# Kernel tuning notes

Hardware: AMD Instinct MI355X
Metric: run time of the kernel (lower is better)

Reference implementation:

```python
import jax, jax.numpy as jnp
import numpy as np

EMBED_DIM = 1024
CONTEXT_DIM = 768
NUM_HEADS = 16
HEAD_DIM = EMBED_DIM // NUM_HEADS
B, N, M = 8, 4096, 77


def setup_inputs() -> dict:
    key = jax.random.key(0)
    ks = jax.random.split(key, 12)
    s_in = 1.0 / np.sqrt(EMBED_DIM)
    s_ctx = 1.0 / np.sqrt(CONTEXT_DIM)
    x = jax.random.normal(ks[0], (B, N, EMBED_DIM), dtype=jnp.float32)
    context = jax.random.normal(ks[1], (B, M, CONTEXT_DIM), dtype=jnp.float32)
    # realistic padding mask: each example has a random valid prefix length in [1, M]
    lengths = jax.random.randint(ks[2], (B,), 1, M + 1)
    context_mask = jnp.arange(M)[None, :] < lengths[:, None]  # (B, M) bool
    Wq = jax.random.uniform(ks[3], (EMBED_DIM, EMBED_DIM), jnp.float32, -s_in, s_in)
    bq = jax.random.uniform(ks[4], (EMBED_DIM,), jnp.float32, -s_in, s_in)
    Wk = jax.random.uniform(ks[5], (CONTEXT_DIM, EMBED_DIM), jnp.float32, -s_ctx, s_ctx)
    bk = jax.random.uniform(ks[6], (EMBED_DIM,), jnp.float32, -s_ctx, s_ctx)
    Wv = jax.random.uniform(ks[7], (CONTEXT_DIM, EMBED_DIM), jnp.float32, -s_ctx, s_ctx)
    bv = jax.random.uniform(ks[8], (EMBED_DIM,), jnp.float32, -s_ctx, s_ctx)
    Wo = jax.random.uniform(ks[9], (EMBED_DIM, EMBED_DIM), jnp.float32, -s_in, s_in)
    bo = jax.random.uniform(ks[10], (EMBED_DIM,), jnp.float32, -s_in, s_in)
    return {"x": x, "context": context, "context_mask": context_mask,
            "Wq": Wq, "bq": bq, "Wk": Wk, "bk": bk, "Wv": Wv, "bv": bv,
            "Wo": Wo, "bo": bo}


def reference(x, context, context_mask, Wq, bq, Wk, bk, Wv, bv, Wo, bo):
    H, d = NUM_HEADS, HEAD_DIM
    scale = d ** -0.5
    Bx, Nx, _ = x.shape
    Mx = context.shape[1]
    # projections
    q = (x @ Wq + bq).reshape(Bx, Nx, H, d).transpose(0, 2, 1, 3)        # (B,H,N,d)
    k = (context @ Wk + bk).reshape(Bx, Mx, H, d).transpose(0, 2, 1, 3)  # (B,H,M,d)
    v = (context @ Wv + bv).reshape(Bx, Mx, H, d).transpose(0, 2, 1, 3)  # (B,H,M,d)
    # scores with padding mask
    attn = jnp.einsum('bhnd,bhmd->bhnm', q, k) * scale                   # (B,H,N,M)
    attn = jnp.where(context_mask[:, None, None, :], attn, -jnp.inf)
    attn = jax.nn.softmax(attn, axis=-1)
    out = jnp.einsum('bhnm,bhmd->bhnd', attn, v)                          # (B,H,N,d)
    out = out.transpose(0, 2, 1, 3).reshape(Bx, Nx, H * d)                # (B,N,E)
    return out @ Wo + bo
```

## Files before the change

### kernel.cpp

```cpp
#include <hip/hip_runtime.h>

typedef __bf16 bf16x8 __attribute__((ext_vector_type(8)));
typedef float f32x4 __attribute__((ext_vector_type(4)));

#define EMB 1024
#define CTXD 768
#define NH 16
#define HD 64
#define BB 8
#define NN 4096
#define MM 77
#define MPAD 96

static __device__ __forceinline__ unsigned short f2bf(float f) {
    unsigned u = __builtin_bit_cast(unsigned, f);
    u += 0x7FFFu + ((u >> 16) & 1u);
    return (unsigned short)(u >> 16);
}

__global__ void cast_f32_to_bf16(const float* __restrict__ in,
                                 unsigned short* __restrict__ out, int n8) {
    for (int i = blockIdx.x * blockDim.x + threadIdx.x; i < n8;
         i += gridDim.x * blockDim.x) {
        float4 v0 = ((const float4*)in)[2 * i];
        float4 v1 = ((const float4*)in)[2 * i + 1];
        union { unsigned short u[8]; int4 v; } r;
        r.u[0] = f2bf(v0.x); r.u[1] = f2bf(v0.y);
        r.u[2] = f2bf(v0.z); r.u[3] = f2bf(v0.w);
        r.u[4] = f2bf(v1.x); r.u[5] = f2bf(v1.y);
        r.u[6] = f2bf(v1.z); r.u[7] = f2bf(v1.w);
        ((int4*)out)[i] = r.v;
    }
}

struct PrepArgs {
    const float* wsrc[4];
    unsigned short* wdst[4];
    const float* ctx;
    unsigned short* cbf;
    const unsigned char* mask;
    int* lengths;
    int4* kvzero;
};
__global__ void prep_kernel(PrepArgs pa) {
    const int z = blockIdx.z;
    const int tx = threadIdx.x, ty = threadIdx.y;
    const int tid = ty * 32 + tx;
    if (z < 4) {
        __shared__ float t[32][33];
        int R = (z < 2) ? 1024 : 768, C = 1024;
        int r0 = blockIdx.y * 32;
        if (r0 >= R) return;
        const float* W = pa.wsrc[z];
        unsigned short* Wt = pa.wdst[z];
        int c0 = blockIdx.x * 32;
#pragma unroll
        for (int i = 0; i < 32; i += 8)
            t[ty + i][tx] = W[(size_t)(r0 + ty + i) * C + c0 + tx];
        __syncthreads();
#pragma unroll
        for (int i = 0; i < 32; i += 8)
            Wt[(size_t)(c0 + ty + i) * R + r0 + tx] = f2bf(t[tx][ty + i]);
    } else if (z == 4) {
        int fid = blockIdx.y * 32 + blockIdx.x;
        int i = fid * 256 + tid;
        if (i >= 640 * CTXD / 8) return;
        int row = (i * 8) / CTXD;
        union { unsigned short u[8]; int4 v; } r;
        if (row < BB * MM) {
            float4 v0 = ((const float4*)pa.ctx)[2 * i];
            float4 v1 = ((const float4*)pa.ctx)[2 * i + 1];
            r.u[0] = f2bf(v0.x); r.u[1] = f2bf(v0.y);
            r.u[2] = f2bf(v0.z); r.u[3] = f2bf(v0.w);
            r.u[4] = f2bf(v1.x); r.u[5] = f2bf(v1.y);
            r.u[6] = f2bf(v1.z); r.u[7] = f2bf(v1.w);
        } else {
            r.v = make_int4(0, 0, 0, 0);
        }
        ((int4*)pa.cbf)[i] = r.v;
    } else {
        int fid = blockIdx.y * 32 + blockIdx.x;
        int i = fid * 256 + tid;
        if (i < 196608) pa.kvzero[i] = make_int4(0, 0, 0, 0);
        if (fid == 1023 && tid < 64) {
            int ln = tid;
            int anyOdd = 0, anyF = 0;
            for (int k = ln; k < BB * MM; k += 64) {
                unsigned char v = pa.mask[k];
                if (v == 0x80u || v == 0x3Fu) anyF = 1;
                if ((k & 3) && v) anyOdd = 1;
            }
            anyF = __any(anyF); anyOdd = __any(anyOdd);
            int layout = anyF ? 2 : (anyOdd ? 1 : 0);
            int b = ln >> 3, j = ln & 7, cnt = 0;
            for (int m = j; m < MM; m += 8) {
                int idx = b * MM + m;
                int valid;
                if (layout == 1)      valid = pa.mask[idx] != 0;
                else if (layout == 0) valid = ((const int*)pa.mask)[idx] != 0;
                else                  valid = ((const float*)pa.mask)[idx] != 0.0f;
                cnt += valid ? 1 : 0;
            }
            cnt += __shfl_xor(cnt, 1, 64);
            cnt += __shfl_xor(cnt, 2, 64);
            cnt += __shfl_xor(cnt, 4, 64);
            if (j == 0) pa.lengths[b] = cnt;
        }
    }
}

template <int MODE>
__global__ __launch_bounds__(512, 2) void gemm256_kernel(
    const unsigned short* __restrict__ A, const unsigned short* __restrict__ Bt,
    const float* __restrict__ bias, void* __restrict__ Cout,
    int M, int N, int K) {
    __shared__ unsigned short lds[4][2][256 * 32];
    const int tid = threadIdx.x, wv = tid >> 6, ln = tid & 63;
    const int numN = N >> 8;
    int bid = blockIdx.x;
    const int nwg = (M >> 8) * numN;
    if ((nwg & 7) == 0) { int cpx = nwg >> 3; bid = (bid & 7) * cpx + (bid >> 3); }
    const int nt_ = bid % numN, mt = bid / numN;
    const int m0 = mt << 8, n0 = nt_ << 8;
    const int wr = wv >> 2, wc = wv & 3;
    const int NT = K >> 5;

    const int srow = wv * 16 + (ln >> 2);
    const int sslot = ln & 3;

    auto stageA = [&](int t) {
#pragma unroll
        for (int half = 0; half < 2; ++half) {
            int row = half * 128 + srow;
            int gc = sslot ^ ((row >> 1) & 3);
            __builtin_amdgcn_global_load_lds(
                (const __attribute__((address_space(1))) void*)(
                    A + (size_t)(m0 + row) * K + (t << 5) + gc * 8),
                (__attribute__((address_space(3))) void*)(
                    &lds[t & 3][0][(half * 128 + wv * 16) * 32]),
                16, 0, 0);
        }
    };
    auto stageB = [&](int t) {
#pragma unroll
        for (int half = 0; half < 2; ++half) {
            int row = half * 128 + srow;
            int gc = sslot ^ ((row >> 1) & 3);
            __builtin_amdgcn_global_load_lds(
                (const __attribute__((address_space(1))) void*)(
                    Bt + (size_t)(n0 + row) * K + (t << 5) + gc * 8),
                (__attribute__((address_space(3))) void*)(
                    &lds[t & 3][1][(half * 128 + wv * 16) * 32]),
                16, 0, 0);
        }
    };
    auto readA = [&](const unsigned short* As, int i) -> bf16x8 {
        int arow = wr * 128 + i * 16 + (ln & 15);
        int aslot = (ln >> 4) ^ ((arow >> 1) & 3);
        return *(const bf16x8*)(As + arow * 32 + aslot * 8);
    };
    auto readB = [&](const unsigned short* Bs, int j) -> bf16x8 {
        int brow = wc * 64 + j * 16 + (ln & 15);
        int bslot = (ln >> 4) ^ ((brow >> 1) & 3);
        return *(const bf16x8*)(Bs + brow * 32 + bslot * 8);
    };

    f32x4 acc[8][4] = {};

    stageA(0); stageB(0); stageA(1); stageB(1); stageA(2); stageB(2);
    asm volatile("s_waitcnt vmcnt(8)" ::: "memory");
    __builtin_amdgcn_sched_barrier(0);
    __builtin_amdgcn_s_barrier();

#pragma unroll 4
    for (int t = 0; t < NT; ++t) {
        const unsigned short* As = lds[t & 3][0];
        const unsigned short* Bs = lds[t & 3][1];
        if (t + 3 < NT) stageA(t + 3);
        bf16x8 bfr[4], af[4];
#pragma unroll
        for (int j = 0; j < 4; ++j) bfr[j] = readB(Bs, j);
#pragma unroll
        for (int i = 0; i < 4; ++i) af[i] = readA(As, i);
        __builtin_amdgcn_s_barrier();
        __builtin_amdgcn_s_setprio(1);
#pragma unroll
        for (int i = 0; i < 4; ++i)
#pragma unroll
            for (int j = 0; j < 4; ++j)
                acc[i][j] = __builtin_amdgcn_mfma_f32_16x16x32_bf16(
                    af[i], bfr[j], acc[i][j], 0, 0, 0);
        __builtin_amdgcn_s_setprio(0);
        __builtin_amdgcn_s_barrier();
        if (t + 3 < NT) stageB(t + 3);
#pragma unroll
        for (int i = 0; i < 4; ++i) af[i] = readA(As, i + 4);
        __builtin_amdgcn_s_barrier();
        __builtin_amdgcn_s_setprio(1);
#pragma unroll
        for (int i = 0; i < 4; ++i)
#pragma unroll
            for (int j = 0; j < 4; ++j)
                acc[i + 4][j] = __builtin_amdgcn_mfma_f32_16x16x32_bf16(
                    af[i], bfr[j], acc[i + 4][j], 0, 0, 0);
        __builtin_amdgcn_s_setprio(0);
        if (t < NT - 1) {
            if (t + 3 < NT)      { asm volatile("s_waitcnt vmcnt(8)" ::: "memory"); }
            else if (t + 2 < NT) { asm volatile("s_waitcnt vmcnt(4)" ::: "memory"); }
            else                 { asm volatile("s_waitcnt vmcnt(0)" ::: "memory"); }
            __builtin_amdgcn_sched_barrier(0);
        }
        __builtin_amdgcn_s_barrier();
    }

    float bvals[4];
#pragma unroll
    for (int j = 0; j < 4; ++j)
        bvals[j] = bias[n0 + wc * 64 + j * 16 + (ln & 15)];
#pragma unroll
    for (int i = 0; i < 8; ++i)
#pragma unroll
        for (int j = 0; j < 4; ++j)
#pragma unroll
            for (int r = 0; r < 4; ++r) {
                int row = m0 + wr * 128 + i * 16 + (ln >> 4) * 4 + r;
                int col = n0 + wc * 64 + j * 16 + (ln & 15);
                float v = acc[i][j][r] + bvals[j];
                if constexpr (MODE == 0)
                    ((unsigned short*)Cout)[(size_t)row * N + col] = f2bf(v);
                else
                    ((float*)Cout)[(size_t)row * N + col] = v;
            }
}

static __device__ __forceinline__ void stage_tile(
    const unsigned short* __restrict__ G, int ldg, unsigned short* lds,
    int r0, int kt, int wv, int ln) {
    int rown = ln >> 2;
    int koff = (ln & 3) * 8;
#pragma unroll
    for (int r = 0; r < 2; ++r) {
        int cw = wv * 2 + r;
        const unsigned short* src =
            G + (size_t)(r0 + cw * 16 + rown) * ldg + kt + koff;
        __builtin_amdgcn_global_load_lds(
            (const __attribute__((address_space(1))) void*)src,
            (__attribute__((address_space(3))) void*)(lds + cw * 512),
            16, 0, 0);
    }
}

__global__ __launch_bounds__(256) void gemm_kv_kernel(
    const unsigned short* __restrict__ Cbf,
    const unsigned short* __restrict__ Wk_t, const float* __restrict__ bk,
    unsigned short* __restrict__ Kw,
    const unsigned short* __restrict__ Wv_t, const float* __restrict__ bv,
    unsigned short* __restrict__ Vtw) {
    const int M = 640, N = 1024, K = CTXD;
    __shared__ unsigned short As[128 * 32];
    __shared__ unsigned short Bs[128 * 32];
    const int tid = threadIdx.x, wv = tid >> 6, ln = tid & 63;
    int bid = blockIdx.x;
    const bool isV = bid >= 40;
    if (isV) bid -= 40;
    const unsigned short* Bt = isV ? Wv_t : Wk_t;
    const float* bias = isV ? bv : bk;
    const int numN = N >> 7;
    { int cpx = 5; bid = (bid & 7) * cpx + (bid >> 3); }
    const int nt = bid % numN, mt = bid / numN;
    const int m0 = mt << 7, n0 = nt << 7;
    const int wr = wv >> 1, wc = wv & 1;

    f32x4 acc[4][4] = {};
    for (int kt = 0; kt < K; kt += 32) {
        __syncthreads();
        stage_tile(Cbf, K, As, m0, kt, wv, ln);
        stage_tile(Bt, K, Bs, n0, kt, wv, ln);
        __syncthreads();
        bf16x8 af[4], bfr[4];
#pragma unroll
        for (int i = 0; i < 4; ++i)
            af[i] = *(const bf16x8*)(As + (wr * 64 + i * 16 + (ln & 15)) * 32 +
                                     (ln >> 4) * 8);
#pragma unroll
        for (int j = 0; j < 4; ++j)
            bfr[j] = *(const bf16x8*)(Bs + (wc * 64 + j * 16 + (ln & 15)) * 32 +
                                      (ln >> 4) * 8);
#pragma unroll
        for (int i = 0; i < 4; ++i)
#pragma unroll
            for (int j = 0; j < 4; ++j)
                acc[i][j] = __builtin_amdgcn_mfma_f32_16x16x32_bf16(
                    af[i], bfr[j], acc[i][j], 0, 0, 0);
    }

    float bvals[4];
#pragma unroll
    for (int j = 0; j < 4; ++j)
        bvals[j] = bias[n0 + wc * 64 + j * 16 + (ln & 15)];

#pragma unroll
    for (int i = 0; i < 4; ++i) {
#pragma unroll
        for (int j = 0; j < 4; ++j) {
#pragma unroll
            for (int r = 0; r < 4; ++r) {
                int row = m0 + wr * 64 + i * 16 + (ln >> 4) * 4 + r;
                int col = n0 + wc * 64 + j * 16 + (ln & 15);
                float v = acc[i][j][r] + bvals[j];
                if (row < BB * MM) {
                    int bb = row / MM, m = row - bb * MM;
                    int hh = col >> 6, d = col & 63;
                    if (!isV)
                        Kw[((size_t)(bb * NH + hh) * MPAD + m) * HD + d] = f2bf(v);
                    else
                        Vtw[((size_t)(bb * NH + hh) * HD + d) * MPAD + m] = f2bf(v);
                }
            }
        }
    }
}

__global__ __launch_bounds__(256, 3) void attn_kernel(
    const unsigned short* __restrict__ Q, const unsigned short* __restrict__ Kw,
    const unsigned short* __restrict__ Vt, const int* __restrict__ lengths,
    unsigned short* __restrict__ Out) {
    const int bh = blockIdx.y;
    const int b = bh >> 4, h = bh & 15;
    const int q0 = blockIdx.x * 128;
    const int tid = threadIdx.x, wv = tid >> 6, ln = tid & 63;
    const int len = lengths[b];
    const int kscnt = (len + 31) >> 5;

    __shared__ unsigned short Ps[128][104];

    const unsigned short* Ksrc = Kw + (size_t)bh * (MPAD * HD);
    const unsigned short* Vsrc = Vt + (size_t)bh * (HD * MPAD);

    bf16x8 aq[2][2];
#pragma unroll
    for (int qi = 0; qi < 2; ++qi) {
        const int qr = q0 + wv * 32 + qi * 16 + (ln & 15);
        const unsigned short* qptr =
            Q + (size_t)(b * NN + qr) * EMB + h * HD + (ln >> 4) * 8;
        aq[qi][0] = *(const bf16x8*)(qptr);
        aq[qi][1] = *(const bf16x8*)(qptr + 32);
    }

    bf16x8 vf[3][4];
#pragma unroll
    for (int j = 0; j < 4; ++j)
        vf[0][j] = *(const bf16x8*)(Vsrc + (j * 16 + (ln & 15)) * MPAD +
                                    (ln >> 4) * 8);
    if (kscnt > 1) {
#pragma unroll
        for (int j = 0; j < 4; ++j)
            vf[1][j] = *(const bf16x8*)(Vsrc + (j * 16 + (ln & 15)) * MPAD + 32 +
                                        (ln >> 4) * 8);
    }
    if (kscnt > 2) {
#pragma unroll
        for (int j = 0; j < 4; ++j)
            vf[2][j] = *(const bf16x8*)(Vsrc + (j * 16 + (ln & 15)) * MPAD + 64 +
                                        (ln >> 4) * 8);
    }

    f32x4 s[2][5] = {};
#pragma unroll
    for (int t = 0; t < 5; ++t) {
        if (t * 16 < len) {
            const unsigned short* kp =
                Ksrc + (t * 16 + (ln & 15)) * HD + (ln >> 4) * 8;
            bf16x8 k0 = *(const bf16x8*)(kp);
            bf16x8 k1 = *(const bf16x8*)(kp + 32);
#pragma unroll
            for (int qi = 0; qi < 2; ++qi) {
                s[qi][t] = __builtin_amdgcn_mfma_f32_16x16x32_bf16(
                    aq[qi][0], k0, s[qi][t], 0, 0, 0);
                s[qi][t] = __builtin_amdgcn_mfma_f32_16x16x32_bf16(
                    aq[qi][1], k1, s[qi][t], 0, 0, 0);
            }
        }
    }

    const float scale = 0.125f;
    float mx[2][4], sum[2][4];
#pragma unroll
    for (int qi = 0; qi < 2; ++qi)
#pragma unroll
        for (int r = 0; r < 4; ++r) { mx[qi][r] = -1e30f; sum[qi][r] = 0.f; }
#pragma unroll
    for (int t = 0; t < 5; ++t) {
        int m = t * 16 + (ln & 15);
        bool valid = m < len;
#pragma unroll
        for (int qi = 0; qi < 2; ++qi)
#pragma unroll
            for (int r = 0; r < 4; ++r) {
                float v = valid ? s[qi][t][r] * scale : -1e30f;
                s[qi][t][r] = v;
                mx[qi][r] = fmaxf(mx[qi][r], v);
            }
    }
#pragma unroll
    for (int d = 1; d < 16; d <<= 1)
#pragma unroll
        for (int qi = 0; qi < 2; ++qi)
#pragma unroll
            for (int r = 0; r < 4; ++r)
                mx[qi][r] = fmaxf(mx[qi][r], __shfl_xor(mx[qi][r], d, 64));
#pragma unroll
    for (int t = 0; t < 5; ++t)
#pragma unroll
        for (int qi = 0; qi < 2; ++qi)
#pragma unroll
            for (int r = 0; r < 4; ++r) {
                float p = __expf(s[qi][t][r] - mx[qi][r]);
                s[qi][t][r] = p;
                sum[qi][r] += p;
            }
#pragma unroll
    for (int d = 1; d < 16; d <<= 1)
#pragma unroll
        for (int qi = 0; qi < 2; ++qi)
#pragma unroll
            for (int r = 0; r < 4; ++r)
                sum[qi][r] += __shfl_xor(sum[qi][r], d, 64);

    float rinv[2][4];
#pragma unroll
    for (int qi = 0; qi < 2; ++qi)
#pragma unroll
        for (int r = 0; r < 4; ++r) rinv[qi][r] = 1.0f / sum[qi][r];

#pragma unroll
    for (int t = 0; t < 6; ++t)
#pragma unroll
        for (int qi = 0; qi < 2; ++qi)
#pragma unroll
            for (int r = 0; r < 4; ++r) {
                int row = wv * 32 + qi * 16 + (ln >> 4) * 4 + r;
                float v = (t < 5) ? s[qi][t][r] * rinv[qi][r] : 0.0f;
                Ps[row][t * 16 + (ln & 15)] = f2bf(v);
            }

    f32x4 o[2][4] = {};
    for (int ks = 0; ks < kscnt; ++ks) {
#pragma unroll
        for (int qi = 0; qi < 2; ++qi) {
            bf16x8 pf = *(const bf16x8*)(&Ps[wv * 32 + qi * 16 + (ln & 15)]
                                            [ks * 32 + (ln >> 4) * 8]);
#pragma unroll
            for (int j = 0; j < 4; ++j)
                o[qi][j] = __builtin_amdgcn_mfma_f32_16x16x32_bf16(
                    vf[ks][j], pf, o[qi][j], 0, 0, 0);
        }
    }

#pragma unroll
    for (int qi = 0; qi < 2; ++qi) {
        const int qrow = q0 + wv * 32 + qi * 16 + (ln & 15);
        unsigned short* obase =
            Out + (size_t)(b * NN + qrow) * EMB + h * HD + (ln >> 4) * 4;
#pragma unroll
        for (int j = 0; j < 4; ++j) {
            union { unsigned short u[4]; unsigned long long ll; } pk;
#pragma unroll
            for (int r = 0; r < 4; ++r) pk.u[r] = f2bf(o[qi][j][r]);
            *(unsigned long long*)(obase + j * 16) = pk.ll;
        }
    }
}

extern "C" void kernel_launch(void* const* d_in, const int* in_sizes, int n_in,
                              void* d_out, int out_size, void* d_ws, size_t ws_size,
                              hipStream_t stream) {
    const float* x    = (const float*)d_in[0];
    const float* ctx  = (const float*)d_in[1];
    const unsigned char* cmask = (const unsigned char*)d_in[2];
    const float* Wq = (const float*)d_in[3];
    const float* bq = (const float*)d_in[4];
    const float* Wk = (const float*)d_in[5];
    const float* bk = (const float*)d_in[6];
    const float* Wv = (const float*)d_in[7];
    const float* bv = (const float*)d_in[8];
    const float* Wo = (const float*)d_in[9];
    const float* bo = (const float*)d_in[10];

    char* ws = (char*)d_ws;
    unsigned short* Xbf   = (unsigned short*)(ws);
    unsigned short* Wq_t  = (unsigned short*)(ws + 67108864);
    unsigned short* Wo_t  = (unsigned short*)(ws + 69206016);
    unsigned short* Wk_t  = (unsigned short*)(ws + 71303168);
    unsigned short* Wv_t  = (unsigned short*)(ws + 72876032);
    unsigned short* Cbf   = (unsigned short*)(ws + 74448896);
    unsigned short* Kw    = (unsigned short*)(ws + 75431936);
    unsigned short* Vtw   = (unsigned short*)(ws + 77004800);
    int* lengths          = (int*)(ws + 78577664);
    unsigned short* Qb    = (unsigned short*)d_out;

    PrepArgs pa;
    pa.wsrc[0] = Wq; pa.wsrc[1] = Wo; pa.wsrc[2] = Wk; pa.wsrc[3] = Wv;
    pa.wdst[0] = Wq_t; pa.wdst[1] = Wo_t; pa.wdst[2] = Wk_t; pa.wdst[3] = Wv_t;
    pa.ctx = ctx; pa.cbf = Cbf; pa.mask = cmask; pa.lengths = lengths;
    pa.kvzero = (int4*)Kw;
    prep_kernel<<<dim3(32, 32, 6), dim3(32, 8), 0, stream>>>(pa);

    cast_f32_to_bf16<<<2048, 256, 0, stream>>>(x, Xbf, (BB * NN * EMB) / 8);

    gemm256_kernel<0><<<512, 512, 0, stream>>>(Xbf, Wq_t, bq, Qb, 32768, 1024, 1024);
    gemm_kv_kernel<<<80, 256, 0, stream>>>(Cbf, Wk_t, bk, Kw, Wv_t, bv, Vtw);

    attn_kernel<<<dim3(32, 128), 256, 0, stream>>>(Qb, Kw, Vtw, lengths, Xbf);

    gemm256_kernel<1><<<512, 512, 0, stream>>>(Xbf, Wo_t, bo, d_out, 32768, 1024, 1024);
}
```

Baseline: 293.5 us.

## Fold x cast into prep kernel and merge Q and KV GEMMs into one launch

The fp32-to-bf16 cast of x becomes extra z-slices of the prep kernel. The Q projection GEMM and the small K/V projection GEMM now share one 592-block launch, with the first 80 blocks running the K/V path on 8 waves. This removes two kernel launches and their tail gaps. It also lowers the s_waitcnt vmcnt thresholds in the pipelined GEMMs from 8/4 to 4/2, which waits on more outstanding prefetches than the three-stage-ahead pipeline needs and may reduce load/compute overlap.

```diff
diff --git a/kernel.cpp b/kernel.cpp
--- a/kernel.cpp
+++ b/kernel.cpp
@@ -18,21 +18,6 @@
     return (unsigned short)(u >> 16);
 }
 
-__global__ void cast_f32_to_bf16(const float* __restrict__ in,
-                                 unsigned short* __restrict__ out, int n8) {
-    for (int i = blockIdx.x * blockDim.x + threadIdx.x; i < n8;
-         i += gridDim.x * blockDim.x) {
-        float4 v0 = ((const float4*)in)[2 * i];
-        float4 v1 = ((const float4*)in)[2 * i + 1];
-        union { unsigned short u[8]; int4 v; } r;
-        r.u[0] = f2bf(v0.x); r.u[1] = f2bf(v0.y);
-        r.u[2] = f2bf(v0.z); r.u[3] = f2bf(v0.w);
-        r.u[4] = f2bf(v1.x); r.u[5] = f2bf(v1.y);
-        r.u[6] = f2bf(v1.z); r.u[7] = f2bf(v1.w);
-        ((int4*)out)[i] = r.v;
-    }
-}
-
 struct PrepArgs {
     const float* wsrc[4];
     unsigned short* wdst[4];
@@ -41,6 +26,8 @@
     const unsigned char* mask;
     int* lengths;
     int4* kvzero;
+    const float* x;
+    unsigned short* xbf;
 };
 __global__ void prep_kernel(PrepArgs pa) {
     const int z = blockIdx.z;
@@ -78,7 +65,7 @@
             r.v = make_int4(0, 0, 0, 0);
         }
         ((int4*)pa.cbf)[i] = r.v;
-    } else {
+    } else if (z == 5) {
         int fid = blockIdx.y * 32 + blockIdx.x;
         int i = fid * 256 + tid;
         if (i < 196608) pa.kvzero[i] = make_int4(0, 0, 0, 0);
@@ -106,13 +93,217 @@
             cnt += __shfl_xor(cnt, 4, 64);
             if (j == 0) pa.lengths[b] = cnt;
         }
+    } else {
+        int i = ((z - 6) * 1024 + blockIdx.y * 32 + blockIdx.x) * 256 + tid;
+        float4 v0 = ((const float4*)pa.x)[2 * i];
+        float4 v1 = ((const float4*)pa.x)[2 * i + 1];
+        union { unsigned short u[8]; int4 v; } r;
+        r.u[0] = f2bf(v0.x); r.u[1] = f2bf(v0.y);
+        r.u[2] = f2bf(v0.z); r.u[3] = f2bf(v0.w);
+        r.u[4] = f2bf(v1.x); r.u[5] = f2bf(v1.y);
+        r.u[6] = f2bf(v1.z); r.u[7] = f2bf(v1.w);
+        ((int4*)pa.xbf)[i] = r.v;
     }
 }
 
-template <int MODE>
+__global__ __launch_bounds__(512, 2) void gemm_q_kv(
+    const unsigned short* __restrict__ Xbf, const unsigned short* __restrict__ Wq_t,
+    const float* __restrict__ bq, unsigned short* __restrict__ Qb,
+    const unsigned short* __restrict__ Cbf,
+    const unsigned short* __restrict__ Wk_t, const float* __restrict__ bk,
+    unsigned short* __restrict__ Kw,
+    const unsigned short* __restrict__ Wv_t, const float* __restrict__ bv,
+    unsigned short* __restrict__ Vtw) {
+    __shared__ unsigned short lds[4][2][256 * 32];
+    const int tid = threadIdx.x, wv = tid >> 6, ln = tid & 63;
+    int bid = blockIdx.x;
+
+    if (bid < 80) {
+        const bool isV = bid >= 40;
+        if (isV) bid -= 40;
+        const unsigned short* Bt = isV ? Wv_t : Wk_t;
+        const float* bias = isV ? bv : bk;
+        { int cpx = 5; bid = (bid & 7) * cpx + (bid >> 3); }
+        const int nt = bid & 7, mt = bid >> 3;
+        const int m0 = mt << 7, n0 = nt << 7;
+        const int wr = wv >> 2, wc = wv & 3;
+        unsigned short* As = &lds[0][0][0];
+        unsigned short* Bs = &lds[0][1][0];
+
+        f32x4 acc[4][2] = {};
+        const int rown = ln >> 2, koff = (ln & 3) * 8;
+        for (int kt = 0; kt < CTXD; kt += 32) {
+            __syncthreads();
+            __builtin_amdgcn_global_load_lds(
+                (const __attribute__((address_space(1))) void*)(
+                    Cbf + (size_t)(m0 + wv * 16 + rown) * CTXD + kt + koff),
+                (__attribute__((address_space(3))) void*)(As + wv * 512),
+                16, 0, 0);
+            __builtin_amdgcn_global_load_lds(
+                (const __attribute__((address_space(1))) void*)(
+                    Bt + (size_t)(n0 + wv * 16 + rown) * CTXD + kt + koff),
+                (__attribute__((address_space(3))) void*)(Bs + wv * 512),
+                16, 0, 0);
+            __syncthreads();
+            bf16x8 af[4], bfr[2];
+#pragma unroll
+            for (int i = 0; i < 4; ++i)
+                af[i] = *(const bf16x8*)(As + (wr * 64 + i * 16 + (ln & 15)) * 32 +
+                                         (ln >> 4) * 8);
+#pragma unroll
+            for (int j = 0; j < 2; ++j)
+                bfr[j] = *(const bf16x8*)(Bs + (wc * 32 + j * 16 + (ln & 15)) * 32 +
+                                          (ln >> 4) * 8);
+#pragma unroll
+            for (int i = 0; i < 4; ++i)
+#pragma unroll
+                for (int j = 0; j < 2; ++j)
+                    acc[i][j] = __builtin_amdgcn_mfma_f32_16x16x32_bf16(
+                        af[i], bfr[j], acc[i][j], 0, 0, 0);
+        }
+
+        float bvals[2];
+#pragma unroll
+        for (int j = 0; j < 2; ++j)
+            bvals[j] = bias[n0 + wc * 32 + j * 16 + (ln & 15)];
+#pragma unroll
+        for (int i = 0; i < 4; ++i)
+#pragma unroll
+            for (int j = 0; j < 2; ++j)
+#pragma unroll
+                for (int r = 0; r < 4; ++r) {
+                    int row = m0 + wr * 64 + i * 16 + (ln >> 4) * 4 + r;
+                    int col = n0 + wc * 32 + j * 16 + (ln & 15);
+                    float v = acc[i][j][r] + bvals[j];
+                    if (row < BB * MM) {
+                        int bb = row / MM, m = row - bb * MM;
+                        int hh = col >> 6, d = col & 63;
+                        if (!isV)
+                            Kw[((size_t)(bb * NH + hh) * MPAD + m) * HD + d] = f2bf(v);
+                        else
+                            Vtw[((size_t)(bb * NH + hh) * HD + d) * MPAD + m] = f2bf(v);
+                    }
+                }
+        return;
+    }
+
+    bid -= 80;
+    const int M = 32768, N = 1024, K = 1024;
+    const int numN = N >> 8;
+    const int nwg = (M >> 8) * numN;
+    { int cpx = nwg >> 3; bid = (bid & 7) * cpx + (bid >> 3); }
+    const int nt_ = bid % numN, mt = bid / numN;
+    const int m0 = mt << 8, n0 = nt_ << 8;
+    const int wr = wv >> 2, wc = wv & 3;
+    const int NT = K >> 5;
+
+    const int srow = wv * 16 + (ln >> 2);
+    const int sslot = ln & 3;
+
+    auto stageA = [&](int t) {
+#pragma unroll
+        for (int half = 0; half < 2; ++half) {
+            int row = half * 128 + srow;
+            int gc = sslot ^ ((row >> 1) & 3);
+            __builtin_amdgcn_global_load_lds(
+                (const __attribute__((address_space(1))) void*)(
+                    Xbf + (size_t)(m0 + row) * K + (t << 5) + gc * 8),
+                (__attribute__((address_space(3))) void*)(
+                    &lds[t & 3][0][(half * 128 + wv * 16) * 32]),
+                16, 0, 0);
+        }
+    };
+    auto stageB = [&](int t) {
+#pragma unroll
+        for (int half = 0; half < 2; ++half) {
+            int row = half * 128 + srow;
+            int gc = sslot ^ ((row >> 1) & 3);
+            __builtin_amdgcn_global_load_lds(
+                (const __attribute__((address_space(1))) void*)(
+                    Wq_t + (size_t)(n0 + row) * K + (t << 5) + gc * 8),
+                (__attribute__((address_space(3))) void*)(
+                    &lds[t & 3][1][(half * 128 + wv * 16) * 32]),
+                16, 0, 0);
+        }
+    };
+    auto readA = [&](const unsigned short* As, int i) -> bf16x8 {
+        int arow = wr * 128 + i * 16 + (ln & 15);
+        int aslot = (ln >> 4) ^ ((arow >> 1) & 3);
+        return *(const bf16x8*)(As + arow * 32 + aslot * 8);
+    };
+    auto readB = [&](const unsigned short* Bs, int j) -> bf16x8 {
+        int brow = wc * 64 + j * 16 + (ln & 15);
+        int bslot = (ln >> 4) ^ ((brow >> 1) & 3);
+        return *(const bf16x8*)(Bs + brow * 32 + bslot * 8);
+    };
+
+    f32x4 acc[8][4] = {};
+
+    stageA(0); stageB(0); stageA(1); stageB(1); stageA(2); stageB(2);
+    asm volatile("s_waitcnt vmcnt(8)" ::: "memory");
+    __builtin_amdgcn_sched_barrier(0);
+    __builtin_amdgcn_s_barrier();
+
+#pragma unroll 4
+    for (int t = 0; t < NT; ++t) {
+        const unsigned short* As = lds[t & 3][0];
+        const unsigned short* Bs = lds[t & 3][1];
+        if (t + 3 < NT) stageA(t + 3);
+        bf16x8 bfr[4], af[4];
+#pragma unroll
+        for (int j = 0; j < 4; ++j) bfr[j] = readB(Bs, j);
+#pragma unroll
+        for (int i = 0; i < 4; ++i) af[i] = readA(As, i);
+        __builtin_amdgcn_s_barrier();
+        __builtin_amdgcn_s_setprio(1);
+#pragma unroll
+        for (int i = 0; i < 4; ++i)
+#pragma unroll
+            for (int j = 0; j < 4; ++j)
+                acc[i][j] = __builtin_amdgcn_mfma_f32_16x16x32_bf16(
+                    af[i], bfr[j], acc[i][j], 0, 0, 0);
+        __builtin_amdgcn_s_setprio(0);
+        __builtin_amdgcn_s_barrier();
+        if (t + 3 < NT) stageB(t + 3);
+#pragma unroll
+        for (int i = 0; i < 4; ++i) af[i] = readA(As, i + 4);
+        __builtin_amdgcn_s_barrier();
+        __builtin_amdgcn_s_setprio(1);
+#pragma unroll
+        for (int i = 0; i < 4; ++i)
+#pragma unroll
+            for (int j = 0; j < 4; ++j)
+                acc[i + 4][j] = __builtin_amdgcn_mfma_f32_16x16x32_bf16(
+                    af[i], bfr[j], acc[i + 4][j], 0, 0, 0);
+        __builtin_amdgcn_s_setprio(0);
+        if (t < NT - 1) {
+            if (t + 3 < NT)      { asm volatile("s_waitcnt vmcnt(4)" ::: "memory"); }
+            else if (t + 2 < NT) { asm volatile("s_waitcnt vmcnt(2)" ::: "memory"); }
+            else                 { asm volatile("s_waitcnt vmcnt(0)" ::: "memory"); }
+            __builtin_amdgcn_sched_barrier(0);
+        }
+        __builtin_amdgcn_s_barrier();
+    }
+
+    float bvals[4];
+#pragma unroll
+    for (int j = 0; j < 4; ++j)
+        bvals[j] = bq[n0 + wc * 64 + j * 16 + (ln & 15)];
+#pragma unroll
+    for (int i = 0; i < 8; ++i)
+#pragma unroll
+        for (int j = 0; j < 4; ++j)
+#pragma unroll
+            for (int r = 0; r < 4; ++r) {
+                int row = m0 + wr * 128 + i * 16 + (ln >> 4) * 4 + r;
+                int col = n0 + wc * 64 + j * 16 + (ln & 15);
+                Qb[(size_t)row * N + col] = f2bf(acc[i][j][r] + bvals[j]);
+            }
+}
+
 __global__ __launch_bounds__(512, 2) void gemm256_kernel(
     const unsigned short* __restrict__ A, const unsigned short* __restrict__ Bt,
-    const float* __restrict__ bias, void* __restrict__ Cout,
+    const float* __restrict__ bias, float* __restrict__ Cout,
     int M, int N, int K) {
     __shared__ unsigned short lds[4][2][256 * 32];
     const int tid = threadIdx.x, wv = tid >> 6, ln = tid & 63;
@@ -205,8 +396,8 @@
                     af[i], bfr[j], acc[i + 4][j], 0, 0, 0);
         __builtin_amdgcn_s_setprio(0);
         if (t < NT - 1) {
-            if (t + 3 < NT)      { asm volatile("s_waitcnt vmcnt(8)" ::: "memory"); }
-            else if (t + 2 < NT) { asm volatile("s_waitcnt vmcnt(4)" ::: "memory"); }
+            if (t + 3 < NT)      { asm volatile("s_waitcnt vmcnt(4)" ::: "memory"); }
+            else if (t + 2 < NT) { asm volatile("s_waitcnt vmcnt(2)" ::: "memory"); }
             else                 { asm volatile("s_waitcnt vmcnt(0)" ::: "memory"); }
             __builtin_amdgcn_sched_barrier(0);
         }
@@ -225,100 +416,8 @@
             for (int r = 0; r < 4; ++r) {
                 int row = m0 + wr * 128 + i * 16 + (ln >> 4) * 4 + r;
                 int col = n0 + wc * 64 + j * 16 + (ln & 15);
-                float v = acc[i][j][r] + bvals[j];
-                if constexpr (MODE == 0)
-                    ((unsigned short*)Cout)[(size_t)row * N + col] = f2bf(v);
-                else
-                    ((float*)Cout)[(size_t)row * N + col] = v;
-            }
-}
-
-static __device__ __forceinline__ void stage_tile(
-    const unsigned short* __restrict__ G, int ldg, unsigned short* lds,
-    int r0, int kt, int wv, int ln) {
-    int rown = ln >> 2;
-    int koff = (ln & 3) * 8;
-#pragma unroll
-    for (int r = 0; r < 2; ++r) {
-        int cw = wv * 2 + r;
-        const unsigned short* src =
-            G + (size_t)(r0 + cw * 16 + rown) * ldg + kt + koff;
-        __builtin_amdgcn_global_load_lds(
-            (const __attribute__((address_space(1))) void*)src,
-            (__attribute__((address_space(3))) void*)(lds + cw * 512),
-            16, 0, 0);
-    }
-}
-
-__global__ __launch_bounds__(256) void gemm_kv_kernel(
-    const unsigned short* __restrict__ Cbf,
-    const unsigned short* __restrict__ Wk_t, const float* __restrict__ bk,
-    unsigned short* __restrict__ Kw,
-    const unsigned short* __restrict__ Wv_t, const float* __restrict__ bv,
-    unsigned short* __restrict__ Vtw) {
-    const int M = 640, N = 1024, K = CTXD;
-    __shared__ unsigned short As[128 * 32];
-    __shared__ unsigned short Bs[128 * 32];
-    const int tid = threadIdx.x, wv = tid >> 6, ln = tid & 63;
-    int bid = blockIdx.x;
-    const bool isV = bid >= 40;
-    if (isV) bid -= 40;
-    const unsigned short* Bt = isV ? Wv_t : Wk_t;
-    const float* bias = isV ? bv : bk;
-    const int numN = N >> 7;
-    { int cpx = 5; bid = (bid & 7) * cpx + (bid >> 3); }
-    const int nt = bid % numN, mt = bid / numN;
-    const int m0 = mt << 7, n0 = nt << 7;
-    const int wr = wv >> 1, wc = wv & 1;
-
-    f32x4 acc[4][4] = {};
-    for (int kt = 0; kt < K; kt += 32) {
-        __syncthreads();
-        stage_tile(Cbf, K, As, m0, kt, wv, ln);
-        stage_tile(Bt, K, Bs, n0, kt, wv, ln);
-        __syncthreads();
-        bf16x8 af[4], bfr[4];
-#pragma unroll
-        for (int i = 0; i < 4; ++i)
-            af[i] = *(const bf16x8*)(As + (wr * 64 + i * 16 + (ln & 15)) * 32 +
-                                     (ln >> 4) * 8);
-#pragma unroll
-        for (int j = 0; j < 4; ++j)
-            bfr[j] = *(const bf16x8*)(Bs + (wc * 64 + j * 16 + (ln & 15)) * 32 +
-                                      (ln >> 4) * 8);
-#pragma unroll
-        for (int i = 0; i < 4; ++i)
-#pragma unroll
-            for (int j = 0; j < 4; ++j)
-                acc[i][j] = __builtin_amdgcn_mfma_f32_16x16x32_bf16(
-                    af[i], bfr[j], acc[i][j], 0, 0, 0);
-    }
-
-    float bvals[4];
-#pragma unroll
-    for (int j = 0; j < 4; ++j)
-        bvals[j] = bias[n0 + wc * 64 + j * 16 + (ln & 15)];
-
-#pragma unroll
-    for (int i = 0; i < 4; ++i) {
-#pragma unroll
-        for (int j = 0; j < 4; ++j) {
-#pragma unroll
-            for (int r = 0; r < 4; ++r) {
-                int row = m0 + wr * 64 + i * 16 + (ln >> 4) * 4 + r;
-                int col = n0 + wc * 64 + j * 16 + (ln & 15);
-                float v = acc[i][j][r] + bvals[j];
-                if (row < BB * MM) {
-                    int bb = row / MM, m = row - bb * MM;
-                    int hh = col >> 6, d = col & 63;
-                    if (!isV)
-                        Kw[((size_t)(bb * NH + hh) * MPAD + m) * HD + d] = f2bf(v);
-                    else
-                        Vtw[((size_t)(bb * NH + hh) * HD + d) * MPAD + m] = f2bf(v);
-                }
-            }
-        }
-    }
+                Cout[(size_t)row * N + col] = acc[i][j][r] + bvals[j];
+            }
 }
 
 __global__ __launch_bounds__(256, 3) void attn_kernel(
@@ -504,14 +603,14 @@
     pa.wdst[0] = Wq_t; pa.wdst[1] = Wo_t; pa.wdst[2] = Wk_t; pa.wdst[3] = Wv_t;
     pa.ctx = ctx; pa.cbf = Cbf; pa.mask = cmask; pa.lengths = lengths;
     pa.kvzero = (int4*)Kw;
-    prep_kernel<<<dim3(32, 32, 6), dim3(32, 8), 0, stream>>>(pa);
-
-    cast_f32_to_bf16<<<2048, 256, 0, stream>>>(x, Xbf, (BB * NN * EMB) / 8);
-
-    gemm256_kernel<0><<<512, 512, 0, stream>>>(Xbf, Wq_t, bq, Qb, 32768, 1024, 1024);
-    gemm_kv_kernel<<<80, 256, 0, stream>>>(Cbf, Wk_t, bk, Kw, Wv_t, bv, Vtw);
+    pa.x = x; pa.xbf = Xbf;
+    prep_kernel<<<dim3(32, 32, 22), dim3(32, 8), 0, stream>>>(pa);
+
+    gemm_q_kv<<<592, 512, 0, stream>>>(Xbf, Wq_t, bq, Qb,
+                                       Cbf, Wk_t, bk, Kw, Wv_t, bv, Vtw);
 
     attn_kernel<<<dim3(32, 128), 256, 0, stream>>>(Qb, Kw, Vtw, lengths, Xbf);
 
-    gemm256_kernel<1><<<512, 512, 0, stream>>>(Xbf, Wo_t, bo, d_out, 32768, 1024, 1024);
+    gemm256_kernel<<<512, 512, 0, stream>>>(Xbf, Wo_t, bo, (float*)d_out,
+                                            32768, 1024, 1024);
 }
```

After: 265.0 us. -9.7%, faster.

## Shrink GEMM tiles to 128x128, merge Q and KV GEMMs, fold x cast into prep

Applied to the files above, without the earlier changes.

The 256x256, 512-thread GEMM is replaced by a 128x128, 256-thread variant with a 4-stage LDS pipeline. The Q projection and the small K/V projection now run in one launch, and the fp32-to-bf16 cast of x moves into the prep kernel as extra z-slices. This removes two launches and lets the K/V blocks overlap the Q GEMM, but the smaller tiles lower per-block arithmetic intensity and raise global and LDS traffic per FLOP.

```diff
diff --git a/kernel.cpp b/kernel.cpp
--- a/kernel.cpp
+++ b/kernel.cpp
@@ -18,21 +18,6 @@
     return (unsigned short)(u >> 16);
 }
 
-__global__ void cast_f32_to_bf16(const float* __restrict__ in,
-                                 unsigned short* __restrict__ out, int n8) {
-    for (int i = blockIdx.x * blockDim.x + threadIdx.x; i < n8;
-         i += gridDim.x * blockDim.x) {
-        float4 v0 = ((const float4*)in)[2 * i];
-        float4 v1 = ((const float4*)in)[2 * i + 1];
-        union { unsigned short u[8]; int4 v; } r;
-        r.u[0] = f2bf(v0.x); r.u[1] = f2bf(v0.y);
-        r.u[2] = f2bf(v0.z); r.u[3] = f2bf(v0.w);
-        r.u[4] = f2bf(v1.x); r.u[5] = f2bf(v1.y);
-        r.u[6] = f2bf(v1.z); r.u[7] = f2bf(v1.w);
-        ((int4*)out)[i] = r.v;
-    }
-}
-
 struct PrepArgs {
     const float* wsrc[4];
     unsigned short* wdst[4];
@@ -41,6 +26,8 @@
     const unsigned char* mask;
     int* lengths;
     int4* kvzero;
+    const float* x;
+    unsigned short* xbf;
 };
 __global__ void prep_kernel(PrepArgs pa) {
     const int z = blockIdx.z;
@@ -53,11 +40,11 @@
         if (r0 >= R) return;
         const float* W = pa.wsrc[z];
         unsigned short* Wt = pa.wdst[z];
+#pragma unroll
+        for (int i = 0; i < 32; i += 8)
+            t[ty + i][tx] = W[(size_t)(r0 + ty + i) * C + blockIdx.x * 32 + tx];
+        __syncthreads();
         int c0 = blockIdx.x * 32;
-#pragma unroll
-        for (int i = 0; i < 32; i += 8)
-            t[ty + i][tx] = W[(size_t)(r0 + ty + i) * C + c0 + tx];
-        __syncthreads();
 #pragma unroll
         for (int i = 0; i < 32; i += 8)
             Wt[(size_t)(c0 + ty + i) * R + r0 + tx] = f2bf(t[tx][ty + i]);
@@ -78,7 +65,7 @@
             r.v = make_int4(0, 0, 0, 0);
         }
         ((int4*)pa.cbf)[i] = r.v;
-    } else {
+    } else if (z == 5) {
         int fid = blockIdx.y * 32 + blockIdx.x;
         int i = fid * 256 + tid;
         if (i < 196608) pa.kvzero[i] = make_int4(0, 0, 0, 0);
@@ -106,23 +93,31 @@
             cnt += __shfl_xor(cnt, 4, 64);
             if (j == 0) pa.lengths[b] = cnt;
         }
+    } else {
+        int i = ((z - 6) * 1024 + blockIdx.y * 32 + blockIdx.x) * 256 + tid;
+        float4 v0 = ((const float4*)pa.x)[2 * i];
+        float4 v1 = ((const float4*)pa.x)[2 * i + 1];
+        union { unsigned short u[8]; int4 v; } r;
+        r.u[0] = f2bf(v0.x); r.u[1] = f2bf(v0.y);
+        r.u[2] = f2bf(v0.z); r.u[3] = f2bf(v0.w);
+        r.u[4] = f2bf(v1.x); r.u[5] = f2bf(v1.y);
+        r.u[6] = f2bf(v1.z); r.u[7] = f2bf(v1.w);
+        ((int4*)pa.xbf)[i] = r.v;
     }
 }
 
 template <int MODE>
-__global__ __launch_bounds__(512, 2) void gemm256_kernel(
+static __device__ __forceinline__ void gemm128_core(
     const unsigned short* __restrict__ A, const unsigned short* __restrict__ Bt,
     const float* __restrict__ bias, void* __restrict__ Cout,
-    int M, int N, int K) {
-    __shared__ unsigned short lds[4][2][256 * 32];
-    const int tid = threadIdx.x, wv = tid >> 6, ln = tid & 63;
-    const int numN = N >> 8;
-    int bid = blockIdx.x;
-    const int nwg = (M >> 8) * numN;
+    int M, int N, int K, int bid, int wv, int ln,
+    unsigned short (*lds)[2][128 * 32]) {
+    const int numN = N >> 7;
+    const int nwg = (M >> 7) * numN;
     if ((nwg & 7) == 0) { int cpx = nwg >> 3; bid = (bid & 7) * cpx + (bid >> 3); }
     const int nt_ = bid % numN, mt = bid / numN;
-    const int m0 = mt << 8, n0 = nt_ << 8;
-    const int wr = wv >> 2, wc = wv & 3;
+    const int m0 = mt << 7, n0 = nt_ << 7;
+    const int wr = wv >> 1, wc = wv & 1;
     const int NT = K >> 5;
 
     const int srow = wv * 16 + (ln >> 2);
@@ -131,31 +126,31 @@
     auto stageA = [&](int t) {
 #pragma unroll
         for (int half = 0; half < 2; ++half) {
-            int row = half * 128 + srow;
+            int row = half * 64 + srow;
             int gc = sslot ^ ((row >> 1) & 3);
             __builtin_amdgcn_global_load_lds(
                 (const __attribute__((address_space(1))) void*)(
                     A + (size_t)(m0 + row) * K + (t << 5) + gc * 8),
                 (__attribute__((address_space(3))) void*)(
-                    &lds[t & 3][0][(half * 128 + wv * 16) * 32]),
+                    &lds[t & 3][0][(half * 64 + wv * 16) * 32]),
                 16, 0, 0);
         }
     };
     auto stageB = [&](int t) {
 #pragma unroll
         for (int half = 0; half < 2; ++half) {
-            int row = half * 128 + srow;
+            int row = half * 64 + srow;
             int gc = sslot ^ ((row >> 1) & 3);
             __builtin_amdgcn_global_load_lds(
                 (const __attribute__((address_space(1))) void*)(
                     Bt + (size_t)(n0 + row) * K + (t << 5) + gc * 8),
                 (__attribute__((address_space(3))) void*)(
-                    &lds[t & 3][1][(half * 128 + wv * 16) * 32]),
+                    &lds[t & 3][1][(half * 64 + wv * 16) * 32]),
                 16, 0, 0);
         }
     };
     auto readA = [&](const unsigned short* As, int i) -> bf16x8 {
-        int arow = wr * 128 + i * 16 + (ln & 15);
+        int arow = wr * 64 + i * 16 + (ln & 15);
         int aslot = (ln >> 4) ^ ((arow >> 1) & 3);
         return *(const bf16x8*)(As + arow * 32 + aslot * 8);
     };
@@ -165,7 +160,7 @@
         return *(const bf16x8*)(Bs + brow * 32 + bslot * 8);
     };
 
-    f32x4 acc[8][4] = {};
+    f32x4 acc[4][4] = {};
 
     stageA(0); stageB(0); stageA(1); stageB(1); stageA(2); stageB(2);
     asm volatile("s_waitcnt vmcnt(8)" ::: "memory");
@@ -177,15 +172,14 @@
         const unsigned short* As = lds[t & 3][0];
         const unsigned short* Bs = lds[t & 3][1];
         if (t + 3 < NT) stageA(t + 3);
-        bf16x8 bfr[4], af[4];
+        bf16x8 bfr[4], af[2];
 #pragma unroll
         for (int j = 0; j < 4; ++j) bfr[j] = readB(Bs, j);
-#pragma unroll
-        for (int i = 0; i < 4; ++i) af[i] = readA(As, i);
+        af[0] = readA(As, 0); af[1] = readA(As, 1);
         __builtin_amdgcn_s_barrier();
         __builtin_amdgcn_s_setprio(1);
 #pragma unroll
-        for (int i = 0; i < 4; ++i)
+        for (int i = 0; i < 2; ++i)
 #pragma unroll
             for (int j = 0; j < 4; ++j)
                 acc[i][j] = __builtin_amdgcn_mfma_f32_16x16x32_bf16(
@@ -193,20 +187,19 @@
         __builtin_amdgcn_s_setprio(0);
         __builtin_amdgcn_s_barrier();
         if (t + 3 < NT) stageB(t + 3);
-#pragma unroll
-        for (int i = 0; i < 4; ++i) af[i] = readA(As, i + 4);
+        af[0] = readA(As, 2); af[1] = readA(As, 3);
         __builtin_amdgcn_s_barrier();
         __builtin_amdgcn_s_setprio(1);
 #pragma unroll
-        for (int i = 0; i < 4; ++i)
+        for (int i = 0; i < 2; ++i)
 #pragma unroll
             for (int j = 0; j < 4; ++j)
-                acc[i + 4][j] = __builtin_amdgcn_mfma_f32_16x16x32_bf16(
-                    af[i], bfr[j], acc[i + 4][j], 0, 0, 0);
+                acc[i + 2][j] = __builtin_amdgcn_mfma_f32_16x16x32_bf16(
+                    af[i], bfr[j], acc[i + 2][j], 0, 0, 0);
         __builtin_amdgcn_s_setprio(0);
         if (t < NT - 1) {
-            if (t + 3 < NT)      { asm volatile("s_waitcnt vmcnt(8)" ::: "memory"); }
-            else if (t + 2 < NT) { asm volatile("s_waitcnt vmcnt(4)" ::: "memory"); }
+            if (t + 3 < NT)      { asm volatile("s_waitcnt vmcnt(4)" ::: "memory"); }
+            else if (t + 2 < NT) { asm volatile("s_waitcnt vmcnt(2)" ::: "memory"); }
             else                 { asm volatile("s_waitcnt vmcnt(0)" ::: "memory"); }
             __builtin_amdgcn_sched_barrier(0);
         }
@@ -218,12 +211,12 @@
     for (int j = 0; j < 4; ++j)
         bvals[j] = bias[n0 + wc * 64 + j * 16 + (ln & 15)];
 #pragma unroll
-    for (int i = 0; i < 8; ++i)
+    for (int i = 0; i < 4; ++i)
 #pragma unroll
         for (int j = 0; j < 4; ++j)
 #pragma unroll
             for (int r = 0; r < 4; ++r) {
-                int row = m0 + wr * 128 + i * 16 + (ln >> 4) * 4 + r;
+                int row = m0 + wr * 64 + i * 16 + (ln >> 4) * 4 + r;
                 int col = n0 + wc * 64 + j * 16 + (ln & 15);
                 float v = acc[i][j][r] + bvals[j];
                 if constexpr (MODE == 0)
@@ -233,92 +226,100 @@
             }
 }
 
-static __device__ __forceinline__ void stage_tile(
-    const unsigned short* __restrict__ G, int ldg, unsigned short* lds,
-    int r0, int kt, int wv, int ln) {
-    int rown = ln >> 2;
-    int koff = (ln & 3) * 8;
-#pragma unroll
-    for (int r = 0; r < 2; ++r) {
-        int cw = wv * 2 + r;
-        const unsigned short* src =
-            G + (size_t)(r0 + cw * 16 + rown) * ldg + kt + koff;
-        __builtin_amdgcn_global_load_lds(
-            (const __attribute__((address_space(1))) void*)src,
-            (__attribute__((address_space(3))) void*)(lds + cw * 512),
-            16, 0, 0);
-    }
-}
-
-__global__ __launch_bounds__(256) void gemm_kv_kernel(
+__global__ __launch_bounds__(256) void gemm_q_kv(
+    const unsigned short* __restrict__ Xbf, const unsigned short* __restrict__ Wq_t,
+    const float* __restrict__ bq, unsigned short* __restrict__ Qb,
     const unsigned short* __restrict__ Cbf,
     const unsigned short* __restrict__ Wk_t, const float* __restrict__ bk,
     unsigned short* __restrict__ Kw,
     const unsigned short* __restrict__ Wv_t, const float* __restrict__ bv,
     unsigned short* __restrict__ Vtw) {
-    const int M = 640, N = 1024, K = CTXD;
-    __shared__ unsigned short As[128 * 32];
-    __shared__ unsigned short Bs[128 * 32];
+    __shared__ unsigned short lds[4][2][128 * 32];
     const int tid = threadIdx.x, wv = tid >> 6, ln = tid & 63;
     int bid = blockIdx.x;
-    const bool isV = bid >= 40;
-    if (isV) bid -= 40;
-    const unsigned short* Bt = isV ? Wv_t : Wk_t;
-    const float* bias = isV ? bv : bk;
-    const int numN = N >> 7;
-    { int cpx = 5; bid = (bid & 7) * cpx + (bid >> 3); }
-    const int nt = bid % numN, mt = bid / numN;
-    const int m0 = mt << 7, n0 = nt << 7;
-    const int wr = wv >> 1, wc = wv & 1;
-
-    f32x4 acc[4][4] = {};
-    for (int kt = 0; kt < K; kt += 32) {
-        __syncthreads();
-        stage_tile(Cbf, K, As, m0, kt, wv, ln);
-        stage_tile(Bt, K, Bs, n0, kt, wv, ln);
-        __syncthreads();
-        bf16x8 af[4], bfr[4];
+
+    if (bid < 80) {
+        const bool isV = bid >= 40;
+        if (isV) bid -= 40;
+        const unsigned short* Bt = isV ? Wv_t : Wk_t;
+        const float* bias = isV ? bv : bk;
+        { int cpx = 5; bid = (bid & 7) * cpx + (bid >> 3); }
+        const int nt = bid & 7, mt = bid >> 3;
+        const int m0 = mt << 7, n0 = nt << 7;
+        const int wr = wv >> 1, wc = wv & 1;
+        unsigned short* As = &lds[0][0][0];
+        unsigned short* Bs = &lds[0][1][0];
+
+        f32x4 acc[4][4] = {};
+        const int rown = ln >> 2, koff = (ln & 3) * 8;
+        for (int kt = 0; kt < CTXD; kt += 32) {
+            __syncthreads();
+#pragma unroll
+            for (int r = 0; r < 2; ++r) {
+                int cw = wv * 2 + r;
+                __builtin_amdgcn_global_load_lds(
+                    (const __attribute__((address_space(1))) void*)(
+                        Cbf + (size_t)(m0 + cw * 16 + rown) * CTXD + kt + koff),
+                    (__attribute__((address_space(3))) void*)(As + cw * 512),
+                    16, 0, 0);
+                __builtin_amdgcn_global_load_lds(
+                    (const __attribute__((address_space(1))) void*)(
+                        Bt + (size_t)(n0 + cw * 16 + rown) * CTXD + kt + koff),
+                    (__attribute__((address_space(3))) void*)(Bs + cw * 512),
+                    16, 0, 0);
+            }
+            __syncthreads();
+            bf16x8 af[4], bfr[4];
+#pragma unroll
+            for (int i = 0; i < 4; ++i)
+                af[i] = *(const bf16x8*)(As + (wr * 64 + i * 16 + (ln & 15)) * 32 +
+                                         (ln >> 4) * 8);
+#pragma unroll
+            for (int j = 0; j < 4; ++j)
+                bfr[j] = *(const bf16x8*)(Bs + (wc * 64 + j * 16 + (ln & 15)) * 32 +
+                                          (ln >> 4) * 8);
+#pragma unroll
+            for (int i = 0; i < 4; ++i)
+#pragma unroll
+                for (int j = 0; j < 4; ++j)
+                    acc[i][j] = __builtin_amdgcn_mfma_f32_16x16x32_bf16(
+                        af[i], bfr[j], acc[i][j], 0, 0, 0);
+        }
+
+        float bvals[4];
+#pragma unroll
+        for (int j = 0; j < 4; ++j)
+            bvals[j] = bias[n0 + wc * 64 + j * 16 + (ln & 15)];
 #pragma unroll
         for (int i = 0; i < 4; ++i)
-            af[i] = *(const bf16x8*)(As + (wr * 64 + i * 16 + (ln & 15)) * 32 +
-                                     (ln >> 4) * 8);
-#pragma unroll
-        for (int j = 0; j < 4; ++j)
-            bfr[j] = *(const bf16x8*)(Bs + (wc * 64 + j * 16 + (ln & 15)) * 32 +
-                                      (ln >> 4) * 8);
-#pragma unroll
-        for (int i = 0; i < 4; ++i)
 #pragma unroll
             for (int j = 0; j < 4; ++j)
-                acc[i][j] = __builtin_amdgcn_mfma_f32_16x16x32_bf16(
-                    af[i], bfr[j], acc[i][j], 0, 0, 0);
-    }
-
-    float bvals[4];
-#pragma unroll
-    for (int j = 0; j < 4; ++j)
-        bvals[j] = bias[n0 + wc * 64 + j * 16 + (ln & 15)];
-
-#pragma unroll
-    for (int i = 0; i < 4; ++i) {
-#pragma unroll
-        for (int j = 0; j < 4; ++j) {
-#pragma unroll
-            for (int r = 0; r < 4; ++r) {
-                int row = m0 + wr * 64 + i * 16 + (ln >> 4) * 4 + r;
-                int col = n0 + wc * 64 + j * 16 + (ln & 15);
-                float v = acc[i][j][r] + bvals[j];
-                if (row < BB * MM) {
-                    int bb = row / MM, m = row - bb * MM;
-                    int hh = col >> 6, d = col & 63;
-                    if (!isV)
-                        Kw[((size_t)(bb * NH + hh) * MPAD + m) * HD + d] = f2bf(v);
-                    else
-                        Vtw[((size_t)(bb * NH + hh) * HD + d) * MPAD + m] = f2bf(v);
+#pragma unroll
+                for (int r = 0; r < 4; ++r) {
+                    int row = m0 + wr * 64 + i * 16 + (ln >> 4) * 4 + r;
+                    int col = n0 + wc * 64 + j * 16 + (ln & 15);
+                    float v = acc[i][j][r] + bvals[j];
+                    if (row < BB * MM) {
+                        int bb = row / MM, m = row - bb * MM;
+                        int hh = col >> 6, d = col & 63;
+                        if (!isV)
+                            Kw[((size_t)(bb * NH + hh) * MPAD + m) * HD + d] = f2bf(v);
+                        else
+                            Vtw[((size_t)(bb * NH + hh) * HD + d) * MPAD + m] = f2bf(v);
+                    }
                 }
-            }
-        }
-    }
+        return;
+    }
+
+    gemm128_core<0>(Xbf, Wq_t, bq, Qb, 32768, 1024, 1024, bid - 80, wv, ln, lds);
+}
+
+__global__ __launch_bounds__(256) void gemm128_o(
+    const unsigned short* __restrict__ A, const unsigned short* __restrict__ Bt,
+    const float* __restrict__ bias, float* __restrict__ Cout) {
+    __shared__ unsigned short lds[4][2][128 * 32];
+    const int tid = threadIdx.x, wv = tid >> 6, ln = tid & 63;
+    gemm128_core<1>(A, Bt, bias, Cout, 32768, 1024, 1024, blockIdx.x, wv, ln, lds);
 }
 
 __global__ __launch_bounds__(256, 3) void attn_kernel(
@@ -504,14 +505,13 @@
     pa.wdst[0] = Wq_t; pa.wdst[1] = Wo_t; pa.wdst[2] = Wk_t; pa.wdst[3] = Wv_t;
     pa.ctx = ctx; pa.cbf = Cbf; pa.mask = cmask; pa.lengths = lengths;
     pa.kvzero = (int4*)Kw;
-    prep_kernel<<<dim3(32, 32, 6), dim3(32, 8), 0, stream>>>(pa);
-
-    cast_f32_to_bf16<<<2048, 256, 0, stream>>>(x, Xbf, (BB * NN * EMB) / 8);
-
-    gemm256_kernel<0><<<512, 512, 0, stream>>>(Xbf, Wq_t, bq, Qb, 32768, 1024, 1024);
-    gemm_kv_kernel<<<80, 256, 0, stream>>>(Cbf, Wk_t, bk, Kw, Wv_t, bv, Vtw);
+    pa.x = x; pa.xbf = Xbf;
+    prep_kernel<<<dim3(32, 32, 22), dim3(32, 8), 0, stream>>>(pa);
+
+    gemm_q_kv<<<2128, 256, 0, stream>>>(Xbf, Wq_t, bq, Qb,
+                                        Cbf, Wk_t, bk, Kw, Wv_t, bv, Vtw);
 
     attn_kernel<<<dim3(32, 128), 256, 0, stream>>>(Qb, Kw, Vtw, lengths, Xbf);
 
-    gemm256_kernel<1><<<512, 512, 0, stream>>>(Xbf, Wo_t, bo, d_out, 32768, 1024, 1024);
-}
+    gemm128_o<<<2048, 256, 0, stream>>>(Xbf, Wo_t, bo, (float*)d_out);
+}
```

Result: faster. 278.7 us (-5.0%).
